# Kernel optimization log

Hardware: AMD Instinct MI355X
Metric: run time of the kernel (lower is better)

Reference implementation:

```python
import jax, jax.numpy as jnp
import numpy as np

T = 65536
OBS_DIM = 64
ACTION_DIM = 16
EMB_DIM = 8  # min(action_dim, 8)
HID = 256
NOBJ = 4
IN_DIM = OBS_DIM + EMB_DIM


def setup_inputs() -> dict:
    key = jax.random.key(0)
    ks = jax.random.split(key, 16)
    g = lambda k, shape, s=0.05: (jax.random.normal(k, shape, dtype=jnp.float32) * s)
    inp = {
        "observations": jax.random.normal(ks[0], (T, OBS_DIM), dtype=jnp.float32),
        "actions": jax.random.randint(ks[1], (T,), 0, ACTION_DIM),
        "emb": g(ks[2], (ACTION_DIM, EMB_DIM)),
        # layer 0 (input_dim -> hidden)
        "Win0": g(ks[3], (HID, IN_DIM)),
        "WB0": g(ks[4], (HID, IN_DIM)),
        "WC0": g(ks[5], (HID, IN_DIM)),
        "Wd0": g(ks[6], (HID, IN_DIM)),
        "Alog0": jax.random.normal(ks[7], (HID,), dtype=jnp.float32),
        # layer 1 (hidden -> hidden)
        "Win1": g(ks[8], (HID, HID)),
        "WB1": g(ks[9], (HID, HID)),
        "WC1": g(ks[10], (HID, HID)),
        "Wd1": g(ks[11], (HID, HID)),
        "Alog1": jax.random.normal(ks[12], (HID,), dtype=jnp.float32),
        # output head
        "Wout": g(ks[13], (NOBJ, HID)),
        "bout": jnp.zeros((NOBJ,), dtype=jnp.float32),
    }
    return inp


def _ssm_layer(x, Win, WB, WC, Wd, Alog):
    """One selective-SSM layer: h_t = exp(delta_t * A) * h_{t-1} + B_t * x_state_t; y = C * h."""
    x_state = x @ Win.T            # [T, H]
    B = x @ WB.T                   # [T, H]
    C = x @ WC.T                   # [T, H]
    delta = jax.nn.sigmoid(x @ Wd.T)  # [T, H]
    A = -jnp.exp(Alog)             # [H]
    A_bar = jnp.exp(delta * A)     # [T, H], decay factors
    Bx = B * x_state               # [T, H], inputs to the recurrence

    def step(h, inputs):
        a, bx = inputs
        h = a * h + bx
        return h, h

    h0 = jnp.zeros((x_state.shape[-1],), dtype=x_state.dtype)
    _, h_seq = jax.lax.scan(step, h0, (A_bar, Bx))
    return C * h_seq


def reference(observations, actions, emb,
              Win0, WB0, WC0, Wd0, Alog0,
              Win1, WB1, WC1, Wd1, Alog1,
              Wout, bout):
    x = jnp.concatenate([observations, emb[actions]], axis=-1)  # [T, IN_DIM]
    x = _ssm_layer(x, Win0, WB0, WC0, Wd0, Alog0)
    x = _ssm_layer(x, Win1, WB1, WC1, Wd1, Alog1)
    out = x @ Wout.T + bout                                     # [T, NOBJ]
    return jax.nn.softplus(out) + 1.0
```

## Files before the change

### kernel.cpp

```cpp
#include <hip/hip_runtime.h>

typedef unsigned short u16;
typedef __attribute__((ext_vector_type(8))) short bf16x8;
typedef __attribute__((ext_vector_type(4))) float f32x4;
typedef __attribute__((ext_vector_type(8))) unsigned short u16x8;

#define T_LEN 65536
#define HID 256
#define K0 96
#define K1 256
#define BM 128
#define BN 128
#define CHUNK 64
#define NCHUNK 1024
#define NSEG 32
#define CPS 32

__device__ __forceinline__ float bf2f(u16 u) {
  unsigned x = ((unsigned)u) << 16; float f; __builtin_memcpy(&f, &x, 4); return f;
}
__device__ __forceinline__ u16 f2bf(float f) {
  unsigned x; __builtin_memcpy(&x, &f, 4);
  x += 0x7FFFu + ((x >> 16) & 1u);
  return (u16)(x >> 16);
}

__device__ __forceinline__ void gl_lds16(const void* g, void* l) {
  __builtin_amdgcn_global_load_lds((const __attribute__((address_space(1))) unsigned int*)g,
                                   (__attribute__((address_space(3))) unsigned int*)l,
                                   16, 0, 0);
}

__global__ __launch_bounds__(256) void build_x0(
    const float* __restrict__ obs, const int* __restrict__ act,
    const float* __restrict__ emb, u16* __restrict__ x0)
{
  const int idx = blockIdx.x * 256 + threadIdx.x;
  const int t = idx / 24, seg = idx - t * 24;
  u16 v0 = 0, v1 = 0, v2 = 0, v3 = 0;
  if (seg < 16) {
    const float4 f = *(const float4*)&obs[(size_t)t * 64 + seg * 4];
    v0 = f2bf(f.x); v1 = f2bf(f.y); v2 = f2bf(f.z); v3 = f2bf(f.w);
  } else if (seg < 18) {
    const int a = act[t];
    const int e0 = (seg - 16) * 4;
    v0 = f2bf(emb[a * 8 + e0 + 0]); v1 = f2bf(emb[a * 8 + e0 + 1]);
    v2 = f2bf(emb[a * 8 + e0 + 2]); v3 = f2bf(emb[a * 8 + e0 + 3]);
  }
  u16* p = &x0[(size_t)t * 96 + seg * 4];
  p[0] = v0; p[1] = v1; p[2] = v2; p[3] = v3;
}

__global__ __launch_bounds__(256) void prep_w(
    const float* __restrict__ Win0, const float* __restrict__ WB0,
    const float* __restrict__ WC0,  const float* __restrict__ Wd0,
    const float* __restrict__ Alog0,
    const float* __restrict__ Win1, const float* __restrict__ WB1,
    const float* __restrict__ WC1,  const float* __restrict__ Wd1,
    const float* __restrict__ Alog1,
    u16* __restrict__ W0v, u16* __restrict__ W1v, float* __restrict__ Aneg)
{
  const int idx = blockIdx.x * 256 + threadIdx.x;
  if (idx < 1024 * K0) {
    const int row = idx / K0, k = idx - row * K0;
    const int h = row >> 2, p = row & 3;
    const float* W = (p == 0) ? Win0 : (p == 1) ? WB0 : (p == 2) ? WC0 : Wd0;
    W0v[idx] = f2bf((k < 72) ? W[h * 72 + k] : 0.f);
  } else if (idx < 1024 * K0 + 1024 * K1) {
    const int j = idx - 1024 * K0;
    const int row = j >> 8, k = j & 255;
    const int h = row >> 2, p = row & 3;
    const float* W = (p == 0) ? Win1 : (p == 1) ? WB1 : (p == 2) ? WC1 : Wd1;
    W1v[j] = f2bf(W[h * 256 + k]);
  } else if (idx < 1024 * K0 + 1024 * K1 + 512) {
    const int j = idx - (1024 * K0 + 1024 * K1);
    Aneg[j] = -__expf((j < 256) ? Alog0[j] : Alog1[j - 256]);
  }
}

template <int KDIM>
__global__ __launch_bounds__(256, 3) void gemm_scan(
    const u16* __restrict__ X, const u16* __restrict__ Wv,
    const float* __restrict__ Aneg,
    unsigned* __restrict__ uvb,
    float* __restrict__ aprod, float* __restrict__ hlast)
{
  static_assert(KDIM % 32 == 0, "K must be multiple of 32");
  __shared__ u16 sA[BM * 32];
  __shared__ u16 sB[BN * 32];
  __shared__ float sT[64 * 132];
  __shared__ float sAgg[8 * 32 * 2];

  const int tid = threadIdx.x;
  const int l   = tid & 63;
  const int w   = tid >> 6;
  const int bid = blockIdx.x;
  const int xcd = bid & 7;
  const int k_  = bid >> 3;
  const int mt  = xcd * 64 + (k_ >> 3);
  const int nt  = k_ & 7;
  const int m0  = mt * BM;
  const int n0  = nt * BN;
  const int wm  = (w >> 1) * 64;
  const int wn  = (w & 1) * 64;

  f32x4 acc[4][4];
  const f32x4 zero = {0.f, 0.f, 0.f, 0.f};
#pragma unroll
  for (int mi = 0; mi < 4; ++mi)
#pragma unroll
    for (int ni = 0; ni < 4; ++ni) acc[mi][ni] = zero;

  const int rr = w * 32 + (l >> 2);
  const int kb = (l & 3) * 16;

  for (int ks = 0; ks < KDIM / 32; ++ks) {
    __syncthreads();
#pragma unroll
    for (int i = 0; i < 2; ++i) {
      const char* gA = (const char*)(X + (size_t)(m0 + rr + i * 16) * KDIM + ks * 32) + kb;
      gl_lds16(gA, (char*)sA + w * 2048 + i * 1024);
      const char* gB = (const char*)(Wv + (size_t)(n0 + rr + i * 16) * KDIM + ks * 32) + kb;
      gl_lds16(gB, (char*)sB + w * 2048 + i * 1024);
    }
    __syncthreads();

    bf16x8 af[4], bfr[4];
#pragma unroll
    for (int mi = 0; mi < 4; ++mi)
      af[mi] = *(const bf16x8*)&sA[(wm + mi * 16 + (l & 15)) * 32 + (l >> 4) * 8];
#pragma unroll
    for (int ni = 0; ni < 4; ++ni)
      bfr[ni] = *(const bf16x8*)&sB[(wn + ni * 16 + (l & 15)) * 32 + (l >> 4) * 8];
#pragma unroll
    for (int mi = 0; mi < 4; ++mi)
#pragma unroll
      for (int ni = 0; ni < 4; ++ni)
        acc[mi][ni] = __builtin_amdgcn_mfma_f32_16x16x32_bf16(af[mi], bfr[ni], acc[mi][ni], 0, 0, 0);
  }

  const int q  = tid >> 5;
  const int c  = tid & 31;
  const int ch = (n0 >> 2) + c;
  const float An = Aneg[ch];

  for (int hh = 0; hh < 2; ++hh) {
    __syncthreads();
    if ((w >> 1) == hh) {
#pragma unroll
      for (int mi = 0; mi < 4; ++mi)
#pragma unroll
        for (int ni = 0; ni < 4; ++ni)
#pragma unroll
          for (int v = 0; v < 4; ++v)
            sT[(mi * 16 + (l >> 4) * 4 + v) * 132 + wn + ni * 16 + (l & 15)] = acc[mi][ni][v];
    }
    __syncthreads();

    float Pl[8], Hl[8], Cl[8];
    float ap = 1.f, hl = 0.f;
#pragma unroll
    for (int j = 0; j < 8; ++j) {
      const int tl = q * 8 + j;
      const float pin = sT[tl * 132 + 4 * c + 0];
      const float pB  = sT[tl * 132 + 4 * c + 1];
      const float pC  = sT[tl * 132 + 4 * c + 2];
      const float pd  = sT[tl * 132 + 4 * c + 3];
      const float delta = 1.f / (1.f + __expf(-pd));
      const float a  = __expf(delta * An);
      hl = a * hl + pB * pin;
      ap *= a;
      Pl[j] = ap; Hl[j] = hl; Cl[j] = pC;
    }
    sAgg[(q * 32 + c) * 2 + 0] = ap;
    sAgg[(q * 32 + c) * 2 + 1] = hl;
    __syncthreads();

    float sap = 1.f, shl = 0.f;
    for (int qq = 0; qq < q; ++qq) {
      const float a_ = sAgg[(qq * 32 + c) * 2 + 0];
      const float h_ = sAgg[(qq * 32 + c) * 2 + 1];
      shl = a_ * shl + h_;
      sap *= a_;
    }
#pragma unroll
    for (int j = 0; j < 8; ++j) {
      const int tl = q * 8 + j;
      const float hloc = Hl[j] + Pl[j] * shl;
      const float vpfx = Pl[j] * sap;
      const unsigned pack = (unsigned)f2bf(Cl[j] * hloc)
                          | ((unsigned)f2bf(Cl[j] * vpfx) << 16);
      uvb[(size_t)(m0 + hh * 64 + tl) * HID + ch] = pack;
    }
    if (q == 7) {
      const int chunk = mt * 2 + hh;
      aprod[(size_t)chunk * HID + ch] = sap * ap;
      hlast[(size_t)chunk * HID + ch] = Hl[7] + Pl[7] * shl;
    }
  }
}

__global__ __launch_bounds__(256) void pass2a(
    const float* __restrict__ aprod, const float* __restrict__ hlast,
    float* __restrict__ clocal, float* __restrict__ apfxc,
    float* __restrict__ segAP, float* __restrict__ segHL)
{
  const int s = blockIdx.x;
  const int h = threadIdx.x;
  float H = 0.f, P = 1.f;
#pragma unroll 4
  for (int j = 0; j < CPS; ++j) {
    const size_t o = (size_t)(s * CPS + j) * HID + h;
    clocal[o] = H; apfxc[o] = P;
    const float a = aprod[o], hh = hlast[o];
    H = a * H + hh;
    P *= a;
  }
  segAP[s * HID + h] = P;
  segHL[s * HID + h] = H;
}

__global__ __launch_bounds__(256) void pass2b(
    const float* __restrict__ segAP, const float* __restrict__ segHL,
    float* __restrict__ segc)
{
  const int h = threadIdx.x;
  float S = 0.f;
#pragma unroll 4
  for (int s = 0; s < NSEG; ++s) {
    segc[s * HID + h] = S;
    S = segAP[s * HID + h] * S + segHL[s * HID + h];
  }
}

__global__ __launch_bounds__(256) void combine(
    const unsigned* __restrict__ uvb,
    const float* __restrict__ clocal, const float* __restrict__ apfxc,
    const float* __restrict__ segc, u16* __restrict__ y)
{
  const size_t vi = (size_t)blockIdx.x * 256 + threadIdx.x;
  const int t   = (int)(vi >> 5);
  const int ch0 = ((int)vi & 31) * 8;
  const int ck  = t >> 6;
  const int sg  = ck / CPS;
  const float* cl = &clocal[(size_t)ck * HID + ch0];
  const float* ax = &apfxc[(size_t)ck * HID + ch0];
  const float* sc = &segc[(size_t)sg * HID + ch0];
  const float4 cl0 = *(const float4*)&cl[0], cl1 = *(const float4*)&cl[4];
  const float4 ax0 = *(const float4*)&ax[0], ax1 = *(const float4*)&ax[4];
  const float4 sc0 = *(const float4*)&sc[0], sc1 = *(const float4*)&sc[4];
  const float crv[8] = {
    cl0.x + ax0.x * sc0.x, cl0.y + ax0.y * sc0.y,
    cl0.z + ax0.z * sc0.z, cl0.w + ax0.w * sc0.w,
    cl1.x + ax1.x * sc1.x, cl1.y + ax1.y * sc1.y,
    cl1.z + ax1.z * sc1.z, cl1.w + ax1.w * sc1.w };
  const uint4 p0 = *(const uint4*)&uvb[vi * 8];
  const uint4 p1 = *(const uint4*)&uvb[vi * 8 + 4];
  const unsigned pk[8] = {p0.x, p0.y, p0.z, p0.w, p1.x, p1.y, p1.z, p1.w};
  u16x8 o;
#pragma unroll
  for (int j = 0; j < 8; ++j)
    o[j] = f2bf(bf2f((u16)(pk[j] & 0xffffu)) + bf2f((u16)(pk[j] >> 16)) * crv[j]);
  *(u16x8*)&y[vi * 8] = o;
}

__global__ __launch_bounds__(256) void head(
    const u16* __restrict__ y1, const float* __restrict__ Wout,
    const float* __restrict__ bout, float* __restrict__ out)
{
  __shared__ u16 ly[64 * 264];
  __shared__ float lw[4 * HID];
  __shared__ float lb[4];
  const int tid = threadIdx.x;
  for (int i = tid; i < 4 * HID; i += 256) lw[i] = Wout[i];
  if (tid < 4) lb[tid] = bout[tid];
  const size_t rbase = (size_t)blockIdx.x * 64 * HID;
#pragma unroll
  for (int i = 0; i < 8; ++i) {
    const int lin = i * 256 + tid;
    const int r = lin >> 5, c8 = lin & 31;
    *(u16x8*)&ly[r * 264 + c8 * 8] = *(const u16x8*)&y1[rbase + (size_t)r * HID + c8 * 8];
  }
  __syncthreads();
  const int t = tid >> 2, o = tid & 3;
  float acc = lb[o];
#pragma unroll 8
  for (int h = 0; h < HID; ++h)
    acc += bf2f(ly[t * 264 + h]) * lw[o * HID + h];
  out[((size_t)blockIdx.x * 64 + t) * 4 + o] = logf(1.f + __expf(acc)) + 1.f;
}

extern "C" void kernel_launch(void* const* d_in, const int* in_sizes, int n_in,
                              void* d_out, int out_size, void* d_ws, size_t ws_size,
                              hipStream_t stream)
{
  (void)in_sizes; (void)n_in; (void)out_size; (void)ws_size;
  const float* obs   = (const float*)d_in[0];
  const int*   act   = (const int*)d_in[1];
  const float* emb   = (const float*)d_in[2];
  const float* Win0  = (const float*)d_in[3];
  const float* WB0   = (const float*)d_in[4];
  const float* WC0   = (const float*)d_in[5];
  const float* Wd0   = (const float*)d_in[6];
  const float* Alog0 = (const float*)d_in[7];
  const float* Win1  = (const float*)d_in[8];
  const float* WB1   = (const float*)d_in[9];
  const float* WC1   = (const float*)d_in[10];
  const float* Wd1   = (const float*)d_in[11];
  const float* Alog1 = (const float*)d_in[12];
  const float* Wout  = (const float*)d_in[13];
  const float* bout  = (const float*)d_in[14];
  float* out = (float*)d_out;

  char* ws = (char*)d_ws;
  size_t off = 0;
  auto alloc = [&](size_t bytes) {
    char* p = ws + off;
    off += (bytes + 255) & ~(size_t)255;
    return p;
  };
  u16*      x0    = (u16*)     alloc((size_t)T_LEN * K0 * 2);
  u16*      W0v   = (u16*)     alloc((size_t)1024 * K0 * 2);
  u16*      W1v   = (u16*)     alloc((size_t)1024 * K1 * 2);
  float*    Aneg  = (float*)   alloc(512 * 4);
  unsigned* uvb   = (unsigned*)alloc((size_t)T_LEN * HID * 4);
  u16*      y     = (u16*)     alloc((size_t)T_LEN * HID * 2);
  float*    aprod = (float*)   alloc((size_t)NCHUNK * HID * 4);
  float*    hlast = (float*)   alloc((size_t)NCHUNK * HID * 4);
  float*    clocal= (float*)   alloc((size_t)NCHUNK * HID * 4);
  float*    apfxc = (float*)   alloc((size_t)NCHUNK * HID * 4);
  float*    segAP = (float*)   alloc((size_t)NSEG * HID * 4);
  float*    segHL = (float*)   alloc((size_t)NSEG * HID * 4);
  float*    segc  = (float*)   alloc((size_t)NSEG * HID * 4);

  build_x0<<<T_LEN * 24 / 256, 256, 0, stream>>>(obs, act, emb, x0);
  prep_w<<<(1024 * K0 + 1024 * K1 + 512 + 255) / 256, 256, 0, stream>>>(
      Win0, WB0, WC0, Wd0, Alog0, Win1, WB1, WC1, Wd1, Alog1, W0v, W1v, Aneg);

  gemm_scan<K0><<<4096, 256, 0, stream>>>(x0, W0v, Aneg, uvb, aprod, hlast);
  pass2a<<<NSEG, 256, 0, stream>>>(aprod, hlast, clocal, apfxc, segAP, segHL);
  pass2b<<<1, 256, 0, stream>>>(segAP, segHL, segc);
  combine<<<T_LEN * HID / 8 / 256, 256, 0, stream>>>(uvb, clocal, apfxc, segc, y);

  gemm_scan<K1><<<4096, 256, 0, stream>>>(y, W1v, Aneg + 256, uvb, aprod, hlast);
  pass2a<<<NSEG, 256, 0, stream>>>(aprod, hlast, clocal, apfxc, segAP, segHL);
  pass2b<<<1, 256, 0, stream>>>(segAP, segHL, segc);
  combine<<<T_LEN * HID / 8 / 256, 256, 0, stream>>>(uvb, clocal, apfxc, segc, y);

  head<<<T_LEN / 64, 256, 0, stream>>>(y, Wout, bout, out);
}
```

Baseline: 261.0 us.

## Double-buffer GEMM K-loop with async LDS loads and alias scan buffer

Replaces the single-buffered global-to-LDS load loop with a two-stage ping-pong buffer, so the next K slice is prefetched while MFMAs run on the current one. Explicit vmcnt and lgkmcnt waits with raw barriers replace the __syncthreads pairs. The transpose scratch buffer now aliases the GEMM staging memory, which cuts LDS use and allows occupancy to go from 3 to 4 blocks per CU. The scan also reads the four projections with one 16-byte vector load instead of four scalar loads. Risks are register pressure under the tighter launch bound and correctness of the hand-written wait counts.

```diff
diff --git a/kernel.cpp b/kernel.cpp
--- a/kernel.cpp
+++ b/kernel.cpp
@@ -79,17 +79,17 @@
 }
 
 template <int KDIM>
-__global__ __launch_bounds__(256, 3) void gemm_scan(
+__global__ __launch_bounds__(256, 4) void gemm_scan(
     const u16* __restrict__ X, const u16* __restrict__ Wv,
     const float* __restrict__ Aneg,
     unsigned* __restrict__ uvb,
     float* __restrict__ aprod, float* __restrict__ hlast)
 {
   static_assert(KDIM % 32 == 0, "K must be multiple of 32");
-  __shared__ u16 sA[BM * 32];
-  __shared__ u16 sB[BN * 32];
-  __shared__ float sT[64 * 132];
+  constexpr int NK = KDIM / 32;
+  __shared__ alignas(16) char smem[33792];
   __shared__ float sAgg[8 * 32 * 2];
+  float* sT = (float*)smem;
 
   const int tid = threadIdx.x;
   const int l   = tid & 63;
@@ -114,17 +114,31 @@
   const int rr = w * 32 + (l >> 2);
   const int kb = (l & 3) * 16;
 
-  for (int ks = 0; ks < KDIM / 32; ++ks) {
-    __syncthreads();
-#pragma unroll
-    for (int i = 0; i < 2; ++i) {
-      const char* gA = (const char*)(X + (size_t)(m0 + rr + i * 16) * KDIM + ks * 32) + kb;
-      gl_lds16(gA, (char*)sA + w * 2048 + i * 1024);
-      const char* gB = (const char*)(Wv + (size_t)(n0 + rr + i * 16) * KDIM + ks * 32) + kb;
-      gl_lds16(gB, (char*)sB + w * 2048 + i * 1024);
-    }
-    __syncthreads();
-
+#define STAGE(KS, BUF)                                                          \
+  {                                                                             \
+    _Pragma("unroll")                                                           \
+    for (int i = 0; i < 2; ++i) {                                               \
+      const char* gA = (const char*)(X + (size_t)(m0 + rr + i * 16) * KDIM + (KS) * 32) + kb; \
+      gl_lds16(gA, smem + (BUF) * 16384 + w * 2048 + i * 1024);                 \
+      const char* gB = (const char*)(Wv + (size_t)(n0 + rr + i * 16) * KDIM + (KS) * 32) + kb; \
+      gl_lds16(gB, smem + (BUF) * 16384 + 8192 + w * 2048 + i * 1024);          \
+    }                                                                           \
+  }
+
+  STAGE(0, 0);
+  int cur = 0;
+  for (int ks = 0; ks < NK; ++ks) {
+    if (ks + 1 < NK) {
+      STAGE(ks + 1, cur ^ 1);
+      asm volatile("s_waitcnt vmcnt(4)" ::: "memory");
+    } else {
+      asm volatile("s_waitcnt vmcnt(0)" ::: "memory");
+    }
+    __builtin_amdgcn_s_barrier();
+    asm volatile("" ::: "memory");
+
+    const u16* sA = (const u16*)(smem + cur * 16384);
+    const u16* sB = (const u16*)(smem + cur * 16384 + 8192);
     bf16x8 af[4], bfr[4];
 #pragma unroll
     for (int mi = 0; mi < 4; ++mi)
@@ -137,6 +151,11 @@
 #pragma unroll
       for (int ni = 0; ni < 4; ++ni)
         acc[mi][ni] = __builtin_amdgcn_mfma_f32_16x16x32_bf16(af[mi], bfr[ni], acc[mi][ni], 0, 0, 0);
+
+    asm volatile("s_waitcnt lgkmcnt(0)" ::: "memory");
+    __builtin_amdgcn_s_barrier();
+    asm volatile("" ::: "memory");
+    cur ^= 1;
   }
 
   const int q  = tid >> 5;
@@ -162,15 +181,12 @@
 #pragma unroll
     for (int j = 0; j < 8; ++j) {
       const int tl = q * 8 + j;
-      const float pin = sT[tl * 132 + 4 * c + 0];
-      const float pB  = sT[tl * 132 + 4 * c + 1];
-      const float pC  = sT[tl * 132 + 4 * c + 2];
-      const float pd  = sT[tl * 132 + 4 * c + 3];
-      const float delta = 1.f / (1.f + __expf(-pd));
+      const f32x4 pv = *(const f32x4*)&sT[tl * 132 + 4 * c];
+      const float delta = 1.f / (1.f + __expf(-pv[3]));
       const float a  = __expf(delta * An);
-      hl = a * hl + pB * pin;
+      hl = a * hl + pv[1] * pv[0];
       ap *= a;
-      Pl[j] = ap; Hl[j] = hl; Cl[j] = pC;
+      Pl[j] = ap; Hl[j] = hl; Cl[j] = pv[2];
     }
     sAgg[(q * 32 + c) * 2 + 0] = ap;
     sAgg[(q * 32 + c) * 2 + 1] = hl;
@@ -198,6 +214,7 @@
       hlast[(size_t)chunk * HID + ch] = Hl[7] + Pl[7] * shl;
     }
   }
+#undef STAGE
 }
 
 __global__ __launch_bounds__(256) void pass2a(
```

Result: slower. 274.8 us (+5.3%).

## Load GEMM fragments directly from global into registers with double buffering

Applied to the files above, without the earlier changes.

Removes the LDS staging buffers for the GEMM operands. Each wave now loads its bf16x8 MFMA fragments straight from global memory into registers, with a two-stage register double buffer and the k-loop fully unrolled, which drops two barriers per k-step. The scan epilogue also replaces four scalar LDS reads with one vectorized f32x4 read. The trade-off is that operand tiles are no longer shared across waves through LDS, so each X and W row is fetched redundantly by two waves. The extra buffers also raise register pressure and could lower occupancy.

```diff
diff --git a/kernel.cpp b/kernel.cpp
--- a/kernel.cpp
+++ b/kernel.cpp
@@ -23,12 +23,6 @@
   unsigned x; __builtin_memcpy(&x, &f, 4);
   x += 0x7FFFu + ((x >> 16) & 1u);
   return (u16)(x >> 16);
-}
-
-__device__ __forceinline__ void gl_lds16(const void* g, void* l) {
-  __builtin_amdgcn_global_load_lds((const __attribute__((address_space(1))) unsigned int*)g,
-                                   (__attribute__((address_space(3))) unsigned int*)l,
-                                   16, 0, 0);
 }
 
 __global__ __launch_bounds__(256) void build_x0(
@@ -86,8 +80,7 @@
     float* __restrict__ aprod, float* __restrict__ hlast)
 {
   static_assert(KDIM % 32 == 0, "K must be multiple of 32");
-  __shared__ u16 sA[BM * 32];
-  __shared__ u16 sB[BN * 32];
+  constexpr int NK = KDIM / 32;
   __shared__ float sT[64 * 132];
   __shared__ float sAgg[8 * 32 * 2];
 
@@ -111,33 +104,37 @@
 #pragma unroll
     for (int ni = 0; ni < 4; ++ni) acc[mi][ni] = zero;
 
-  const int rr = w * 32 + (l >> 2);
-  const int kb = (l & 3) * 16;
-
-  for (int ks = 0; ks < KDIM / 32; ++ks) {
-    __syncthreads();
-#pragma unroll
-    for (int i = 0; i < 2; ++i) {
-      const char* gA = (const char*)(X + (size_t)(m0 + rr + i * 16) * KDIM + ks * 32) + kb;
-      gl_lds16(gA, (char*)sA + w * 2048 + i * 1024);
-      const char* gB = (const char*)(Wv + (size_t)(n0 + rr + i * 16) * KDIM + ks * 32) + kb;
-      gl_lds16(gB, (char*)sB + w * 2048 + i * 1024);
-    }
-    __syncthreads();
-
-    bf16x8 af[4], bfr[4];
-#pragma unroll
-    for (int mi = 0; mi < 4; ++mi)
-      af[mi] = *(const bf16x8*)&sA[(wm + mi * 16 + (l & 15)) * 32 + (l >> 4) * 8];
-#pragma unroll
-    for (int ni = 0; ni < 4; ++ni)
-      bfr[ni] = *(const bf16x8*)&sB[(wn + ni * 16 + (l & 15)) * 32 + (l >> 4) * 8];
-#pragma unroll
-    for (int mi = 0; mi < 4; ++mi)
-#pragma unroll
-      for (int ni = 0; ni < 4; ++ni)
-        acc[mi][ni] = __builtin_amdgcn_mfma_f32_16x16x32_bf16(af[mi], bfr[ni], acc[mi][ni], 0, 0, 0);
-  }
+  const u16* Abase = X  + (size_t)(m0 + wm + (l & 15)) * KDIM + (l >> 4) * 8;
+  const u16* Bbase = Wv + (size_t)(n0 + wn + (l & 15)) * KDIM + (l >> 4) * 8;
+
+  bf16x8 aR[2][4], bR[2][4];
+#define LOADF(BUF, KS)                                                       \
+  {                                                                          \
+    _Pragma("unroll")                                                        \
+    for (int f = 0; f < 4; ++f) {                                            \
+      aR[BUF][f] = *(const bf16x8*)(Abase + (size_t)f * 16 * KDIM + (KS) * 32); \
+      bR[BUF][f] = *(const bf16x8*)(Bbase + (size_t)f * 16 * KDIM + (KS) * 32); \
+    }                                                                        \
+  }
+#define MFMA_ALL(BUF)                                                        \
+  {                                                                          \
+    _Pragma("unroll")                                                        \
+    for (int mi = 0; mi < 4; ++mi)                                           \
+      _Pragma("unroll")                                                      \
+      for (int ni = 0; ni < 4; ++ni)                                         \
+        acc[mi][ni] = __builtin_amdgcn_mfma_f32_16x16x32_bf16(               \
+            aR[BUF][mi], bR[BUF][ni], acc[mi][ni], 0, 0, 0);                 \
+  }
+
+  LOADF(0, 0);
+#pragma unroll
+  for (int ks = 0; ks < NK; ++ks) {
+    const int cur = ks & 1;
+    if (ks + 1 < NK) LOADF(cur ^ 1, ks + 1);
+    MFMA_ALL(cur);
+  }
+#undef LOADF
+#undef MFMA_ALL
 
   const int q  = tid >> 5;
   const int c  = tid & 31;
@@ -162,15 +159,12 @@
 #pragma unroll
     for (int j = 0; j < 8; ++j) {
       const int tl = q * 8 + j;
-      const float pin = sT[tl * 132 + 4 * c + 0];
-      const float pB  = sT[tl * 132 + 4 * c + 1];
-      const float pC  = sT[tl * 132 + 4 * c + 2];
-      const float pd  = sT[tl * 132 + 4 * c + 3];
-      const float delta = 1.f / (1.f + __expf(-pd));
+      const f32x4 pv = *(const f32x4*)&sT[tl * 132 + 4 * c];
+      const float delta = 1.f / (1.f + __expf(-pv[3]));
       const float a  = __expf(delta * An);
-      hl = a * hl + pB * pin;
+      hl = a * hl + pv[1] * pv[0];
       ap *= a;
-      Pl[j] = ap; Hl[j] = hl; Cl[j] = pC;
+      Pl[j] = ap; Hl[j] = hl; Cl[j] = pv[2];
     }
     sAgg[(q * 32 + c) * 2 + 0] = ap;
     sAgg[(q * 32 + c) * 2 + 1] = hl;
```

Result: slower. 334.0 us (+28.0%).
